# Performance work log

Hardware: AMD Instinct MI355X
Metric: run time of the kernel (lower is better)

The kernel has to match this reference:

```python
import jax, jax.numpy as jnp
import numpy as np

N, E, ORDER, D, RANK = 4096, 16384, 3, 13, 128
NUM_PARAMS = ORDER + 1  # BT mode: ids = edge_types[:, i] in [0, order+1)
NUM_ITERS = 3
ATOMS = 7


def setup_inputs() -> dict:
    key = jax.random.key(0)
    ks = jax.random.split(key, 9)
    nodes = jax.random.normal(ks[0], (N, D), dtype=jnp.float32)
    edges = jax.random.randint(ks[1], (E, ORDER), 0, N)
    edge_types = jax.random.randint(ks[2], (E, ORDER), 0, NUM_PARAMS)
    atoms = jax.random.randint(ks[3], (E,), 0, ATOMS)
    atom_edges = jax.random.randint(ks[4], (E, ORDER), 0, ATOMS)
    # BPNet.params / bias: uniform(-1/sqrt(rank), 1/sqrt(rank))
    s1 = 1.0 / np.sqrt(RANK).astype(np.float32)
    bp_params = jax.random.uniform(ks[5], (NUM_PARAMS, D, RANK), minval=-s1, maxval=s1, dtype=jnp.float32)
    bp_bias = jax.random.uniform(ks[6], (NUM_PARAMS, 1, RANK), minval=-s1, maxval=s1, dtype=jnp.float32)
    # HighorderNet params per slot i: [NUM_PARAMS, hidden=RANK, out=D], uniform(-1/sqrt(D), 1/sqrt(D))
    s2 = 1.0 / np.sqrt(D).astype(np.float32)
    ho_params = jax.random.uniform(ks[7], (ORDER, NUM_PARAMS, RANK, D), minval=-s2, maxval=s2, dtype=jnp.float32)
    ho_bias = jax.random.uniform(ks[8], (ORDER, NUM_PARAMS, 1, D), minval=-s2, maxval=s2, dtype=jnp.float32)
    return {"nodes": nodes, "bp_params": bp_params, "bp_bias": bp_bias,
            "ho_params": ho_params, "ho_bias": ho_bias,
            "edges": edges, "edge_types": edge_types, "atoms": atoms, "atom_edges": atom_edges}


def _forward(nodes, bp_params, bp_bias, ho_params, ho_bias, edges, edge_types):
    n_nodes = nodes.shape[0]
    order = edges.shape[1]
    # Stage 1: per-slot gathered matmul rnodes @ W[edge_type] + b, then relu.
    rn = nodes[edges]                        # [E, order, D]
    W = bp_params[edge_types]                # [E, order, D, RANK]
    b = bp_bias[edge_types][:, :, 0, :]      # [E, order, RANK]
    t = jax.nn.relu(jnp.einsum('eod,eodr->eor', rn, W) + b)
    t = jnp.transpose(t, (1, 0, 2))          # [order, E, RANK]
    # Iterated message passing. NOTE: original loop re-reads the same
    # transform_cat each iteration (it is never updated), so every iteration
    # recomputes identical node_msg; we keep the loop for structural fidelity.
    node_msg = jnp.zeros((n_nodes, nodes.shape[1]), nodes.dtype)
    for _ in range(NUM_ITERS):
        node_msg = jnp.zeros((n_nodes, nodes.shape[1]), nodes.dtype)
        for i in range(order):
            # leave-one-out product over the other slots -> [E, RANK]
            others = [t[j] for j in range(order) if j != i]
            fact = others[0]
            for o in others[1:]:
                fact = fact * o
            Wi = ho_params[i][edge_types[:, i]]      # [E, RANK, D]
            bi = ho_bias[i][edge_types[:, i], 0]     # [E, D]
            msg = jnp.einsum('er,erd->ed', fact, Wi) + bi
            # dense one-hot incidence matmul == scatter-add over target nodes
            node_msg = node_msg + jax.ops.segment_sum(msg, edges[:, i], num_segments=n_nodes)
    return node_msg


def reference(nodes, bp_params, bp_bias, ho_params, ho_bias, edges, edge_types, atoms, atom_edges):
    # atoms / atom_edges unused in 'BT' mode (kept for signature fidelity)
    return _forward(nodes, bp_params, bp_bias, ho_params, ho_bias, edges, edge_types)
```

## Files before the change

### kernel.cpp

```cpp
#include <hip/hip_runtime.h>


#define DD 13
#define OD 3
#define NP 4
#define RK 128

typedef unsigned int uint;
typedef _Float16 h2 __attribute__((ext_vector_type(2)));

#define W2H_OFF 0
#define W2H_N   (12 * 13 * 64)
#define W1A_OFF (W2H_OFF + W2H_N)
#define W1A_N   (4 * 7 * 64)
#define W1B_OFF (W1A_OFF + W1A_N)
#define W1B_N   (4 * 7 * 64)
#define B1A_OFF (W1B_OFF + W1B_N)
#define B1A_N   (4 * 64)
#define B1B_OFF (B1A_OFF + B1A_N)
#define B1B_N   (4 * 64)
#define HOB_OFF (B1B_OFF + B1B_N)
#define HOB_N   (12 * 16)
#define TAB_N   (HOB_OFF + HOB_N)
#define NROW_OFF TAB_N
#define NROW_N  (8 * 12 * 8)
#define SH_N    (TAB_N + NROW_N)

__device__ __forceinline__ uint pk(float lo, float hi) {
    return __builtin_bit_cast(uint, __builtin_amdgcn_cvt_pkrtz(lo, hi));
}
__device__ __forceinline__ h2 ash2(uint w) { return __builtin_bit_cast(h2, w); }

template <int CTRL>
__device__ __forceinline__ float dpp_add(float x) {
    int p = __builtin_amdgcn_update_dpp(0, __float_as_int(x), CTRL, 0xF, 0xF, false);
    return x + __int_as_float(p);
}
__device__ __forceinline__ float row_sum16(float x) {
    x = dpp_add<0xB1>(x);
    x = dpp_add<0x4E>(x);
    x = dpp_add<0x141>(x);
    x = dpp_add<0x140>(x);
    return x;
}

__global__ __launch_bounds__(256) void bpnet_pack(
    const float* __restrict__ bp_params,
    const float* __restrict__ bp_bias,
    const float* __restrict__ ho_params,
    const float* __restrict__ ho_bias,
    uint* __restrict__ ws,
    uint* __restrict__ outz, int out_n)
{
    const int tid = blockIdx.x * 256 + threadIdx.x;
    const int nthr = gridDim.x * 256;

    const int n4 = out_n >> 2;
    for (int k = tid; k < n4; k += nthr) ((uint4*)outz)[k] = uint4{0, 0, 0, 0};
    if (tid < (out_n & 3)) outz[(n4 << 2) + tid] = 0;

    if (tid < W1A_OFF) {
        const int c = tid & 63, q = tid >> 6;
        const int dd = q % 13, it = q / 13;
        ws[tid] = pk(ho_params[(size_t)(it * RK + 2 * c) * DD + dd],
                     ho_params[(size_t)(it * RK + 2 * c + 1) * DD + dd]);
    } else if (tid < W1B_OFF) {
        const int j = tid - W1A_OFF;
        const int c = j & 63, q = j >> 6;
        const int p = q % 7, ty = q / 7;
        const int r = 8 * (c >> 2) + (c & 3);
        const float a = bp_params[(ty * DD + 2 * p) * RK + r];
        const float b = (2 * p + 1 < DD) ? bp_params[(ty * DD + 2 * p + 1) * RK + r] : 0.f;
        ws[tid] = pk(a, b);
    } else if (tid < B1A_OFF) {
        const int j = tid - W1B_OFF;
        const int c = j & 63, q = j >> 6;
        const int p = q % 7, ty = q / 7;
        const int r = 8 * (c >> 2) + 4 + (c & 3);
        const float a = bp_params[(ty * DD + 2 * p) * RK + r];
        const float b = (2 * p + 1 < DD) ? bp_params[(ty * DD + 2 * p + 1) * RK + r] : 0.f;
        ws[tid] = pk(a, b);
    } else if (tid < B1B_OFF) {
        const int j = tid - B1A_OFF;
        const int c = j & 63, ty = j >> 6;
        ((float*)ws)[tid] = bp_bias[ty * RK + 8 * (c >> 2) + (c & 3)];
    } else if (tid < HOB_OFF) {
        const int j = tid - B1B_OFF;
        const int c = j & 63, ty = j >> 6;
        ((float*)ws)[tid] = bp_bias[ty * RK + 8 * (c >> 2) + 4 + (c & 3)];
    } else if (tid < TAB_N) {
        const int j = tid - HOB_OFF;
        const int dd = j & 15, it = j >> 4;
        ((float*)ws)[tid] = (dd < DD) ? ho_bias[it * DD + dd] : 0.f;
    }
}

__global__ __launch_bounds__(512, 4) void bpnet_fused(
    const float* __restrict__ nodes,
    const int*   __restrict__ edges,
    const int*   __restrict__ edge_types,
    const uint*  __restrict__ tab,
    float*       __restrict__ out)
{
    __shared__ __align__(16) uint sh[SH_N];
    const int tid  = threadIdx.x;
    const int lane = tid & 63;
    const int wv   = tid >> 6;
    const int e4   = lane >> 4;
    const int g    = lane & 15;
    const int eb   = (blockIdx.x * 8 + wv) * 4;

    int ev = 0, tv = 0;
    if (lane < 12) {
        ev = edges[eb * OD + lane];
        tv = edge_types[eb * OD + lane];
    }

    uint* mynr = sh + NROW_OFF + wv * 96;
#pragma unroll
    for (int pass = 0; pass < 2; ++pass) {
        const int idx = pass * 64 + lane;
        if (idx < 96) {
            const int r = idx >> 3, p = idx & 7;
            const int nr_ = __shfl(ev, r, 64);
            uint v = 0;
            if (p < 6)       v = pk(nodes[(size_t)nr_ * DD + 2 * p],
                                    nodes[(size_t)nr_ * DD + 2 * p + 1]);
            else if (p == 6) v = pk(nodes[(size_t)nr_ * DD + 12], 0.f);
            mynr[r * 8 + p] = v;
        }
    }

    for (int k4 = tid; k4 < TAB_N / 4; k4 += 512)
        ((uint4*)sh)[k4] = ((const uint4*)tab)[k4];
    __syncthreads();

    int tg[OD], et[OD];
#pragma unroll
    for (int i = 0; i < OD; ++i) {
        tg[i] = __shfl(ev, e4 * OD + i, 64);
        et[i] = __shfl(tv, e4 * OD + i, 64);
    }

    float t[OD][8];
#pragma unroll
    for (int o = 0; o < OD; ++o) {
        const uint* nh = mynr + (e4 * OD + o) * 8;
        const uint4 n0 = *(const uint4*)(nh);
        const uint4 n1 = *(const uint4*)(nh + 4);
        const float4 b0 = *(const float4*)((const float*)(sh + B1A_OFF) + et[o] * 64 + 4 * g);
        const float4 b1 = *(const float4*)((const float*)(sh + B1B_OFF) + et[o] * 64 + 4 * g);
        float s[8] = {b0.x, b0.y, b0.z, b0.w, b1.x, b1.y, b1.z, b1.w};
        const uint* wa = sh + W1A_OFF + (et[o] * 7) * 64 + 4 * g;
        const uint* wb = sh + W1B_OFF + (et[o] * 7) * 64 + 4 * g;
#define S1(p, nv) { const uint4 wA = *(const uint4*)(wa + (p) * 64);          \
                    const uint4 wB = *(const uint4*)(wb + (p) * 64);          \
            const h2 nn = ash2(nv);                                           \
            s[0] = __builtin_amdgcn_fdot2(nn, ash2(wA.x), s[0], false);       \
            s[1] = __builtin_amdgcn_fdot2(nn, ash2(wA.y), s[1], false);       \
            s[2] = __builtin_amdgcn_fdot2(nn, ash2(wA.z), s[2], false);       \
            s[3] = __builtin_amdgcn_fdot2(nn, ash2(wA.w), s[3], false);       \
            s[4] = __builtin_amdgcn_fdot2(nn, ash2(wB.x), s[4], false);       \
            s[5] = __builtin_amdgcn_fdot2(nn, ash2(wB.y), s[5], false);       \
            s[6] = __builtin_amdgcn_fdot2(nn, ash2(wB.z), s[6], false);       \
            s[7] = __builtin_amdgcn_fdot2(nn, ash2(wB.w), s[7], false); }
        S1(0, n0.x) S1(1, n0.y) S1(2, n0.z) S1(3, n0.w)
        S1(4, n1.x) S1(5, n1.y) S1(6, n1.z)
#undef S1
#pragma unroll
        for (int r = 0; r < 8; ++r) t[o][r] = fmaxf(s[r], 0.f);
    }

#pragma unroll
    for (int i = 0; i < OD; ++i) {
        const int j = (i + 1) % OD, k = (i + 2) % OD;
        uint fh[4];
#pragma unroll
        for (int r = 0; r < 4; ++r)
            fh[r] = pk(t[j][2 * r] * t[k][2 * r], t[j][2 * r + 1] * t[k][2 * r + 1]);
        const int it = i * NP + et[i];
        const uint* wb2 = sh + W2H_OFF + (it * DD) * 64 + 4 * g;
        float c[DD];
#pragma unroll
        for (int dd = 0; dd < DD; ++dd) {
            const uint4 w = *(const uint4*)(wb2 + dd * 64);
            float a = __builtin_amdgcn_fdot2(ash2(fh[0]), ash2(w.x), 0.f, false);
            a = __builtin_amdgcn_fdot2(ash2(fh[1]), ash2(w.y), a, false);
            a = __builtin_amdgcn_fdot2(ash2(fh[2]), ash2(w.z), a, false);
            a = __builtin_amdgcn_fdot2(ash2(fh[3]), ash2(w.w), a, false);
            c[dd] = a;
        }
#pragma unroll
        for (int dd = 0; dd < DD; ++dd) c[dd] = row_sum16(c[dd]);
        float q = c[0];
#pragma unroll
        for (int dd = 1; dd < DD; ++dd) q = (g == dd) ? c[dd] : q;
        q += ((const float*)(sh + HOB_OFF))[it * 16 + g];
        if (g < DD) atomicAdd(out + (size_t)tg[i] * DD + g, q);
    }
}

extern "C" void kernel_launch(void* const* d_in, const int* in_sizes, int n_in,
                              void* d_out, int out_size, void* d_ws, size_t ws_size,
                              hipStream_t stream) {
    const float* nodes      = (const float*)d_in[0];
    const float* bp_params  = (const float*)d_in[1];
    const float* bp_bias    = (const float*)d_in[2];
    const float* ho_params  = (const float*)d_in[3];
    const float* ho_bias    = (const float*)d_in[4];
    const int*   edges      = (const int*)d_in[5];
    const int*   edge_types = (const int*)d_in[6];
    float* out = (float*)d_out;
    uint*  ws  = (uint*)d_ws;

    const int E = in_sizes[5] / OD;

    bpnet_pack<<<(TAB_N + 255) / 256, 256, 0, stream>>>(
        bp_params, bp_bias, ho_params, ho_bias, ws, (uint*)out, out_size);

    bpnet_fused<<<E / 32, 512, 0, stream>>>(nodes, edges, edge_types, ws, out);
}
```

Before: 81.32 us.

## Precompute per-node per-type stage-1 activations, gather them in edge kernel

```diff
diff --git a/kernel.cpp b/kernel.cpp
--- a/kernel.cpp
+++ b/kernel.cpp
@@ -11,20 +11,16 @@
 
 #define W2H_OFF 0
 #define W2H_N   (12 * 13 * 64)
-#define W1A_OFF (W2H_OFF + W2H_N)
-#define W1A_N   (4 * 7 * 64)
-#define W1B_OFF (W1A_OFF + W1A_N)
-#define W1B_N   (4 * 7 * 64)
-#define B1A_OFF (W1B_OFF + W1B_N)
-#define B1A_N   (4 * 64)
-#define B1B_OFF (B1A_OFF + B1A_N)
-#define B1B_N   (4 * 64)
-#define HOB_OFF (B1B_OFF + B1B_N)
+#define HOB_OFF (W2H_OFF + W2H_N)
 #define HOB_N   (12 * 16)
 #define TAB_N   (HOB_OFF + HOB_N)
-#define NROW_OFF TAB_N
-#define NROW_N  (8 * 12 * 8)
-#define SH_N    (TAB_N + NROW_N)
+#define T_OFF   10240
+
+#define L_W1A 0
+#define L_W1B 1792
+#define L_B1A 3584
+#define L_B1B 3840
+#define L_N   4096
 
 __device__ __forceinline__ uint pk(float lo, float hi) {
     return __builtin_bit_cast(uint, __builtin_amdgcn_cvt_pkrtz(lo, hi));
@@ -44,7 +40,8 @@
     return x;
 }
 
-__global__ __launch_bounds__(256) void bpnet_pack(
+__global__ __launch_bounds__(512) void bpnet_prep(
+    const float* __restrict__ nodes,
     const float* __restrict__ bp_params,
     const float* __restrict__ bp_bias,
     const float* __restrict__ ho_params,
@@ -52,57 +49,100 @@
     uint* __restrict__ ws,
     uint* __restrict__ outz, int out_n)
 {
-    const int tid = blockIdx.x * 256 + threadIdx.x;
-    const int nthr = gridDim.x * 256;
+    __shared__ __align__(16) uint sh[L_N];
+    const int tid  = threadIdx.x;
+    const int gtid = blockIdx.x * 512 + tid;
+    const int nthr = gridDim.x * 512;
 
     const int n4 = out_n >> 2;
-    for (int k = tid; k < n4; k += nthr) ((uint4*)outz)[k] = uint4{0, 0, 0, 0};
-    if (tid < (out_n & 3)) outz[(n4 << 2) + tid] = 0;
-
-    if (tid < W1A_OFF) {
-        const int c = tid & 63, q = tid >> 6;
-        const int dd = q % 13, it = q / 13;
-        ws[tid] = pk(ho_params[(size_t)(it * RK + 2 * c) * DD + dd],
-                     ho_params[(size_t)(it * RK + 2 * c + 1) * DD + dd]);
-    } else if (tid < W1B_OFF) {
-        const int j = tid - W1A_OFF;
-        const int c = j & 63, q = j >> 6;
-        const int p = q % 7, ty = q / 7;
-        const int r = 8 * (c >> 2) + (c & 3);
-        const float a = bp_params[(ty * DD + 2 * p) * RK + r];
-        const float b = (2 * p + 1 < DD) ? bp_params[(ty * DD + 2 * p + 1) * RK + r] : 0.f;
-        ws[tid] = pk(a, b);
-    } else if (tid < B1A_OFF) {
-        const int j = tid - W1B_OFF;
-        const int c = j & 63, q = j >> 6;
-        const int p = q % 7, ty = q / 7;
-        const int r = 8 * (c >> 2) + 4 + (c & 3);
-        const float a = bp_params[(ty * DD + 2 * p) * RK + r];
-        const float b = (2 * p + 1 < DD) ? bp_params[(ty * DD + 2 * p + 1) * RK + r] : 0.f;
-        ws[tid] = pk(a, b);
-    } else if (tid < B1B_OFF) {
-        const int j = tid - B1A_OFF;
-        const int c = j & 63, ty = j >> 6;
-        ((float*)ws)[tid] = bp_bias[ty * RK + 8 * (c >> 2) + (c & 3)];
-    } else if (tid < HOB_OFF) {
-        const int j = tid - B1B_OFF;
-        const int c = j & 63, ty = j >> 6;
-        ((float*)ws)[tid] = bp_bias[ty * RK + 8 * (c >> 2) + 4 + (c & 3)];
-    } else if (tid < TAB_N) {
-        const int j = tid - HOB_OFF;
-        const int dd = j & 15, it = j >> 4;
-        ((float*)ws)[tid] = (dd < DD) ? ho_bias[it * DD + dd] : 0.f;
-    }
-}
-
-__global__ __launch_bounds__(512, 4) void bpnet_fused(
-    const float* __restrict__ nodes,
+    for (int k = gtid; k < n4; k += nthr) ((uint4*)outz)[k] = uint4{0, 0, 0, 0};
+    if (gtid < (out_n & 3)) outz[(n4 << 2) + gtid] = 0;
+
+    for (int k = gtid; k < TAB_N; k += nthr) {
+        if (k < HOB_OFF) {
+            const int c = k & 63, q = k >> 6;
+            const int dd = q % 13, it = q / 13;
+            ws[k] = pk(ho_params[(size_t)(it * RK + 2 * c) * DD + dd],
+                       ho_params[(size_t)(it * RK + 2 * c + 1) * DD + dd]);
+        } else {
+            const int j = k - HOB_OFF;
+            const int dd = j & 15, it = j >> 4;
+            ((float*)ws)[k] = (dd < DD) ? ho_bias[it * DD + dd] : 0.f;
+        }
+    }
+
+    for (int k = tid; k < L_N; k += 512) {
+        if (k < L_W1B) {
+            const int c = k & 63, q = k >> 6;
+            const int p = q % 7, ty = q / 7;
+            const int r = 8 * (c >> 2) + (c & 3);
+            const float a = bp_params[(ty * DD + 2 * p) * RK + r];
+            const float b = (2 * p + 1 < DD) ? bp_params[(ty * DD + 2 * p + 1) * RK + r] : 0.f;
+            sh[k] = pk(a, b);
+        } else if (k < L_B1A) {
+            const int j = k - L_W1B;
+            const int c = j & 63, q = j >> 6;
+            const int p = q % 7, ty = q / 7;
+            const int r = 8 * (c >> 2) + 4 + (c & 3);
+            const float a = bp_params[(ty * DD + 2 * p) * RK + r];
+            const float b = (2 * p + 1 < DD) ? bp_params[(ty * DD + 2 * p + 1) * RK + r] : 0.f;
+            sh[k] = pk(a, b);
+        } else if (k < L_B1B) {
+            const int j = k - L_B1A;
+            const int c = j & 63, ty = j >> 6;
+            ((float*)sh)[k] = bp_bias[ty * RK + 8 * (c >> 2) + (c & 3)];
+        } else {
+            const int j = k - L_B1B;
+            const int c = j & 63, ty = j >> 6;
+            ((float*)sh)[k] = bp_bias[ty * RK + 8 * (c >> 2) + 4 + (c & 3)];
+        }
+    }
+    __syncthreads();
+
+    const int lane = tid & 63;
+    const int wv   = tid >> 6;
+    const int ty   = lane >> 4;
+    const int g    = lane & 15;
+    const int nid  = blockIdx.x * 8 + wv;
+
+    const float* nr_ = nodes + (size_t)nid * DD;
+    uint n[7];
+#pragma unroll
+    for (int p = 0; p < 6; ++p) n[p] = pk(nr_[2 * p], nr_[2 * p + 1]);
+    n[6] = pk(nr_[12], 0.f);
+
+    const float4 b0 = *(const float4*)((const float*)sh + L_B1A + ty * 64 + 4 * g);
+    const float4 b1 = *(const float4*)((const float*)sh + L_B1B + ty * 64 + 4 * g);
+    float s[8] = {b0.x, b0.y, b0.z, b0.w, b1.x, b1.y, b1.z, b1.w};
+    const uint* wa = sh + L_W1A + ty * 7 * 64 + 4 * g;
+    const uint* wb = sh + L_W1B + ty * 7 * 64 + 4 * g;
+#pragma unroll
+    for (int p = 0; p < 7; ++p) {
+        const uint4 wA = *(const uint4*)(wa + p * 64);
+        const uint4 wB = *(const uint4*)(wb + p * 64);
+        const h2 nn = ash2(n[p]);
+        s[0] = __builtin_amdgcn_fdot2(nn, ash2(wA.x), s[0], false);
+        s[1] = __builtin_amdgcn_fdot2(nn, ash2(wA.y), s[1], false);
+        s[2] = __builtin_amdgcn_fdot2(nn, ash2(wA.z), s[2], false);
+        s[3] = __builtin_amdgcn_fdot2(nn, ash2(wA.w), s[3], false);
+        s[4] = __builtin_amdgcn_fdot2(nn, ash2(wB.x), s[4], false);
+        s[5] = __builtin_amdgcn_fdot2(nn, ash2(wB.y), s[5], false);
+        s[6] = __builtin_amdgcn_fdot2(nn, ash2(wB.z), s[6], false);
+        s[7] = __builtin_amdgcn_fdot2(nn, ash2(wB.w), s[7], false);
+    }
+    float* tp = (float*)ws + T_OFF + ((size_t)nid * NP + ty) * RK + 8 * g;
+    *(float4*)tp       = float4{fmaxf(s[0], 0.f), fmaxf(s[1], 0.f), fmaxf(s[2], 0.f), fmaxf(s[3], 0.f)};
+    *(float4*)(tp + 4) = float4{fmaxf(s[4], 0.f), fmaxf(s[5], 0.f), fmaxf(s[6], 0.f), fmaxf(s[7], 0.f)};
+}
+
+__global__ __launch_bounds__(512, 4) void bpnet_edge(
+    const float* __restrict__ T,
     const int*   __restrict__ edges,
     const int*   __restrict__ edge_types,
     const uint*  __restrict__ tab,
     float*       __restrict__ out)
 {
-    __shared__ __align__(16) uint sh[SH_N];
+    __shared__ __align__(16) uint sh[TAB_N];
     const int tid  = threadIdx.x;
     const int lane = tid & 63;
     const int wv   = tid >> 6;
@@ -115,60 +155,30 @@
         ev = edges[eb * OD + lane];
         tv = edge_types[eb * OD + lane];
     }
-
-    uint* mynr = sh + NROW_OFF + wv * 96;
-#pragma unroll
-    for (int pass = 0; pass < 2; ++pass) {
-        const int idx = pass * 64 + lane;
-        if (idx < 96) {
-            const int r = idx >> 3, p = idx & 7;
-            const int nr_ = __shfl(ev, r, 64);
-            uint v = 0;
-            if (p < 6)       v = pk(nodes[(size_t)nr_ * DD + 2 * p],
-                                    nodes[(size_t)nr_ * DD + 2 * p + 1]);
-            else if (p == 6) v = pk(nodes[(size_t)nr_ * DD + 12], 0.f);
-            mynr[r * 8 + p] = v;
-        }
+    int tg[OD], et[OD];
+#pragma unroll
+    for (int i = 0; i < OD; ++i) {
+        tg[i] = __shfl(ev, e4 * OD + i, 64);
+        et[i] = __shfl(tv, e4 * OD + i, 64);
+    }
+
+    float4 ta[OD], tb[OD];
+#pragma unroll
+    for (int o = 0; o < OD; ++o) {
+        const float* tp = T + ((size_t)tg[o] * NP + et[o]) * RK + 8 * g;
+        ta[o] = *(const float4*)tp;
+        tb[o] = *(const float4*)(tp + 4);
     }
 
     for (int k4 = tid; k4 < TAB_N / 4; k4 += 512)
         ((uint4*)sh)[k4] = ((const uint4*)tab)[k4];
     __syncthreads();
 
-    int tg[OD], et[OD];
-#pragma unroll
-    for (int i = 0; i < OD; ++i) {
-        tg[i] = __shfl(ev, e4 * OD + i, 64);
-        et[i] = __shfl(tv, e4 * OD + i, 64);
-    }
-
     float t[OD][8];
 #pragma unroll
     for (int o = 0; o < OD; ++o) {
-        const uint* nh = mynr + (e4 * OD + o) * 8;
-        const uint4 n0 = *(const uint4*)(nh);
-        const uint4 n1 = *(const uint4*)(nh + 4);
-        const float4 b0 = *(const float4*)((const float*)(sh + B1A_OFF) + et[o] * 64 + 4 * g);
-        const float4 b1 = *(const float4*)((const float*)(sh + B1B_OFF) + et[o] * 64 + 4 * g);
-        float s[8] = {b0.x, b0.y, b0.z, b0.w, b1.x, b1.y, b1.z, b1.w};
-        const uint* wa = sh + W1A_OFF + (et[o] * 7) * 64 + 4 * g;
-        const uint* wb = sh + W1B_OFF + (et[o] * 7) * 64 + 4 * g;
-#define S1(p, nv) { const uint4 wA = *(const uint4*)(wa + (p) * 64);          \
-                    const uint4 wB = *(const uint4*)(wb + (p) * 64);          \
-            const h2 nn = ash2(nv);                                           \
-            s[0] = __builtin_amdgcn_fdot2(nn, ash2(wA.x), s[0], false);       \
-            s[1] = __builtin_amdgcn_fdot2(nn, ash2(wA.y), s[1], false);       \
-            s[2] = __builtin_amdgcn_fdot2(nn, ash2(wA.z), s[2], false);       \
-            s[3] = __builtin_amdgcn_fdot2(nn, ash2(wA.w), s[3], false);       \
-            s[4] = __builtin_amdgcn_fdot2(nn, ash2(wB.x), s[4], false);       \
-            s[5] = __builtin_amdgcn_fdot2(nn, ash2(wB.y), s[5], false);       \
-            s[6] = __builtin_amdgcn_fdot2(nn, ash2(wB.z), s[6], false);       \
-            s[7] = __builtin_amdgcn_fdot2(nn, ash2(wB.w), s[7], false); }
-        S1(0, n0.x) S1(1, n0.y) S1(2, n0.z) S1(3, n0.w)
-        S1(4, n1.x) S1(5, n1.y) S1(6, n1.z)
-#undef S1
-#pragma unroll
-        for (int r = 0; r < 8; ++r) t[o][r] = fmaxf(s[r], 0.f);
+        t[o][0] = ta[o].x; t[o][1] = ta[o].y; t[o][2] = ta[o].z; t[o][3] = ta[o].w;
+        t[o][4] = tb[o].x; t[o][5] = tb[o].y; t[o][6] = tb[o].z; t[o][7] = tb[o].w;
     }
 
 #pragma unroll
@@ -213,10 +223,12 @@
     float* out = (float*)d_out;
     uint*  ws  = (uint*)d_ws;
 
+    const int N = in_sizes[0] / DD;
     const int E = in_sizes[5] / OD;
 
-    bpnet_pack<<<(TAB_N + 255) / 256, 256, 0, stream>>>(
-        bp_params, bp_bias, ho_params, ho_bias, ws, (uint*)out, out_size);
-
-    bpnet_fused<<<E / 32, 512, 0, stream>>>(nodes, edges, edge_types, ws, out);
-}
+    bpnet_prep<<<N / 8, 512, 0, stream>>>(
+        nodes, bp_params, bp_bias, ho_params, ho_bias, ws, (uint*)out, out_size);
+
+    bpnet_edge<<<E / 32, 512, 0, stream>>>(
+        (const float*)ws + T_OFF, edges, edge_types, ws, out);
+}
```

New measurement: 87.87 us. 8.1% more time.
